# Performance work log

Measured on AMD Instinct MI355X. Metric: run time of the kernel, lower is better.

Reference implementation:

```python
import jax, jax.numpy as jnp
import numpy as np

B, N, D, H, HID, EN = 2, 4096, 128, 4, 32, 16
ALPHA = 0.2           # LeakyReLU slope
NEG = -9e15           # masked_fill value from the original code


def setup_inputs() -> dict:
    key = jax.random.key(0)
    ks = jax.random.split(key, 6)
    fea = jax.random.normal(ks[0], (B, N, D), dtype=jnp.float32)
    # binary dense adjacency (regulon x gene), square here so narrow() is identity
    adj = jax.random.randint(ks[1], (B, N, N), 0, 2).astype(jnp.float32)
    # per-head GAT params (xavier-ish scale)
    W_heads = jax.random.normal(ks[2], (H, D, HID), dtype=jnp.float32) * 0.1
    a_heads = jax.random.normal(ks[3], (H, 2 * HID, 1), dtype=jnp.float32) * 0.1
    W_last = jax.random.normal(ks[4], (H * HID, EN), dtype=jnp.float32) * 0.1
    a_last = jax.random.normal(ks[5], (2 * EN, 1), dtype=jnp.float32) * 0.1
    return {"fea_mats": fea, "adj_mats": adj, "W_heads": W_heads,
            "a_heads": a_heads, "W_last": W_last, "a_last": a_last}


def _gat_layer(x, adj, W, a, concat):
    # x: [N, d_in], adj: [nr, N], W: [d_in, out], a: [2*out, 1]
    out_dim = W.shape[1]
    wh = x @ W                                   # [N, out]
    nr = adj.shape[0]
    wh1 = wh[:nr] @ a[:out_dim]                  # [nr, 1]
    wh2 = wh @ a[out_dim:]                       # [N, 1]
    e = jax.nn.leaky_relu(wh1 + wh2.T, ALPHA)    # [nr, N]
    # _prepare_attentions: mask by adj, weight by adj, fill zeros with -9e15
    att = jnp.where(adj != 0, e * adj, 0.0)
    att = jnp.where(att == 0, NEG, att)
    att = jax.nn.softmax(att, axis=1)
    # the original detaches attention via a numpy roundtrip
    att = jax.lax.stop_gradient(att)
    res = att @ wh                               # [nr, out]
    return jax.nn.elu(res) if concat else res


def reference(fea_mats, adj_mats, W_heads, a_heads, W_last, a_last):
    def per_sample(x, adj):
        # multi-head attention layers (concat=True), vmapped over heads
        heads = jax.vmap(lambda W, a: _gat_layer(x, adj, W, a, True))(W_heads, a_heads)  # [H, N, HID]
        xcat = jnp.transpose(heads, (1, 0, 2)).reshape(x.shape[0], H * HID)  # torch.cat(dim=1)
        nr = adj.shape[0]
        out = _gat_layer(xcat, adj[:, :nr], W_last, a_last, False)  # adj.narrow(1,0,nr)
        return jax.nn.elu(out)  # [N, EN]
    return jax.vmap(per_sample)(fea_mats, adj_mats)  # [B, N, EN]
```

## Files before the change

kernel.cpp:

```cpp
#include <hip/hip_runtime.h>
#include <hip/hip_bf16.h>
#include <stdint.h>

#define B_ 2
#define N_ 4096
#define D_ 128
#define H_ 4
#define HID_ 32
#define EN_ 16
#define ALPHA_ 0.2f
#define S1_ 4
#define S2_ 4
#define LOG2E_ 1.4426950408889634f

typedef __attribute__((ext_vector_type(8))) _Float16 f16x8;
typedef __attribute__((ext_vector_type(4))) float f32x4;
typedef __attribute__((ext_vector_type(8))) unsigned short u16x8;

__device__ __forceinline__ unsigned short f2h(float v) {
    _Float16 h = (_Float16)v;
    return *(unsigned short*)&h;
}

__global__ __launch_bounds__(256) void maskc_kernel(
    const float* __restrict__ adj, unsigned long long* __restrict__ mask)
{
    const int b = blockIdx.y;
    const int i = blockIdx.x * 4 + (threadIdx.x >> 6);
    const int lane = threadIdx.x & 63;
    const float* ar = adj + ((size_t)b * N_ + i) * N_;
    unsigned long long* mrow = mask + ((size_t)b * N_ + i) * 64;
#pragma unroll 4
    for (int c = 0; c < 16; ++c) {
        float4 v = *(const float4*)(ar + c * 256 + lane * 4);
        unsigned long long b0 = __ballot(v.x != 0.f);
        unsigned long long b1 = __ballot(v.y != 0.f);
        unsigned long long b2 = __ballot(v.z != 0.f);
        unsigned long long b3 = __ballot(v.w != 0.f);
        if (lane == 0) {
            ulonglong2 w01 = {b0, b1}, w23 = {b2, b3};
            *(ulonglong2*)(mrow + c * 4) = w01;
            *(ulonglong2*)(mrow + c * 4 + 2) = w23;
        }
    }
}

__global__ __launch_bounds__(256) void proj1_kernel(
    const float* __restrict__ fea, const float* __restrict__ Wh,
    const float* __restrict__ a_heads,
    float* __restrict__ wh1, float* __restrict__ wh2,
    float* __restrict__ cmax1, unsigned short* __restrict__ whTt)
{
    __shared__ float xs[64][132];
    __shared__ float WT[32][132];
    __shared__ float Wa[2][128];
    __shared__ float as_[2 * HID_];
    __shared__ unsigned short ts[32 * 64];
    __shared__ float rmax[64];
    const int b = blockIdx.z, h = blockIdx.y, i0 = blockIdx.x * 64, tid = threadIdx.x;
    const float* Wp = Wh + (size_t)h * D_ * HID_;
    for (int l = tid; l < 1024; l += 256) {
        float4 w4 = *(const float4*)(Wp + l * 4);
        int k = l >> 3, d = (l & 7) * 4;
        WT[d][k] = w4.x; WT[d + 1][k] = w4.y; WT[d + 2][k] = w4.z; WT[d + 3][k] = w4.w;
    }
    if (tid < 2 * HID_) as_[tid] = a_heads[h * 2 * HID_ + tid];
    const float* xp = fea + ((size_t)b * N_ + i0) * D_;
    for (int l = tid; l < 2048; l += 256) {
        int r = l >> 5, k4 = (l & 31) * 4;
        *(float4*)&xs[r][k4] = *(const float4*)(xp + r * D_ + k4);
    }
    __syncthreads();
    {
        const int k = tid & 127, j = tid >> 7;
        const float* wr = Wp + k * HID_;
        const float* aw = &as_[j * HID_];
        float s = 0.f;
#pragma unroll
        for (int d = 0; d < HID_; d += 4) {
            float4 w4 = *(const float4*)(wr + d);
            s += w4.x * aw[d] + w4.y * aw[d + 1] + w4.z * aw[d + 2] + w4.w * aw[d + 3];
        }
        Wa[j][k] = s;
    }
    const int rg = (tid >> 4) * 4, c = tid & 15;
    float a0[4] = {0.f, 0.f, 0.f, 0.f}, a1[4] = {0.f, 0.f, 0.f, 0.f};
#pragma unroll 8
    for (int k = 0; k < D_; k += 4) {
        float4 w0 = *(float4*)&WT[c][k];
        float4 w1 = *(float4*)&WT[c + 16][k];
#pragma unroll
        for (int i = 0; i < 4; ++i) {
            float4 x4 = *(float4*)&xs[rg + i][k];
            a0[i] += x4.x * w0.x + x4.y * w0.y + x4.z * w0.z + x4.w * w0.w;
            a1[i] += x4.x * w1.x + x4.y * w1.y + x4.z * w1.z + x4.w * w1.w;
        }
    }
#pragma unroll
    for (int i = 0; i < 4; ++i) {
        ts[c * 64 + rg + i] = f2h(a0[i]);
        ts[(c + 16) * 64 + rg + i] = f2h(a1[i]);
    }
    __syncthreads();
    {
        const int row = tid >> 2, q = tid & 3;
        float d1 = 0.f, d2 = 0.f;
#pragma unroll
        for (int k = q * 32; k < q * 32 + 32; k += 4) {
            float4 x4 = *(float4*)&xs[row][k];
            float4 u = *(float4*)&Wa[0][k];
            float4 v = *(float4*)&Wa[1][k];
            d1 += x4.x * u.x + x4.y * u.y + x4.z * u.z + x4.w * u.w;
            d2 += x4.x * v.x + x4.y * v.y + x4.z * v.z + x4.w * v.w;
        }
        d1 += __shfl_xor(d1, 1); d1 += __shfl_xor(d1, 2);
        d2 += __shfl_xor(d2, 1); d2 += __shfl_xor(d2, 2);
        if (q == 0) {
            const size_t o = (size_t)(b * H_ + h) * N_ + i0 + row;
            wh1[o] = d1 * LOG2E_;
            wh2[o] = d2 * LOG2E_;
            rmax[row] = d2 * LOG2E_;
        }
    }
    __syncthreads();
    {
        unsigned short* dst = whTt + ((size_t)(b * H_ + h) * 64 + blockIdx.x) * 2048;
        *(u16x8*)(dst + tid * 8) = *(u16x8*)&ts[tid * 8];
    }
    if (tid < 64) {
        float mx = rmax[tid];
#pragma unroll
        for (int off = 32; off; off >>= 1) mx = fmaxf(mx, __shfl_xor(mx, off));
        if (tid == 0) cmax1[(size_t)(b * H_ + h) * 64 + blockIdx.x] = mx;
    }
}

__global__ __launch_bounds__(256, 4) void attn1_kernel(
    const unsigned long long* __restrict__ mask, const unsigned short* __restrict__ whT,
    const float* __restrict__ wh1, const float* __restrict__ wh2,
    const float* __restrict__ cmax1,
    float* __restrict__ x2p, float* __restrict__ l1p)
{
    __shared__ unsigned long long mask_s[32][17];
    const int b = blockIdx.z, split = blockIdx.y, i0 = blockIdx.x * 32;
    const int tid = threadIdx.x, lane = tid & 63, h = tid >> 6;
    const int m = lane & 15, quad = lane >> 4;
    {
        const int r = tid >> 3, w = (tid & 7) * 2;
        ulonglong2 mw = *(const ulonglong2*)(mask + ((size_t)b * N_ + i0 + r) * 64
                                             + split * 16 + w);
        mask_s[r][w] = mw.x; mask_s[r][w + 1] = mw.y;
    }
    const float* cm = cmax1 + (size_t)(b * H_ + h) * 64;
    float Mh = cm[lane];
#pragma unroll
    for (int off = 32; off; off >>= 1) Mh = fmaxf(Mh, __shfl_xor(Mh, off));
    const size_t bhN = (size_t)(b * H_ + h) * N_;
    const float w1r0 = wh1[bhN + i0 + m];
    const float w1r1 = wh1[bhN + i0 + 16 + m];
    const float sb0 = w1r0 + Mh, sb1 = w1r1 + Mh;
    const float mr0 = fmaxf(sb0, ALPHA_ * sb0);
    const float mr1 = fmaxf(sb1, ALPHA_ * sb1);
    const float* wvb = wh2 + bhN + split * 1024 + quad * 8;
    const unsigned short* bpb = whT + (size_t)(b * H_ + h) * 131072
                              + (size_t)split * 16 * 2048 + m * 64 + quad * 8;
    f32x4 a00 = {0.f,0.f,0.f,0.f}, a01 = {0.f,0.f,0.f,0.f}, a02 = {0.f,0.f,0.f,0.f};
    f32x4 a10 = {0.f,0.f,0.f,0.f}, a11 = {0.f,0.f,0.f,0.f}, a12 = {0.f,0.f,0.f,0.f};
    f16x8 ones;
#pragma unroll
    for (int q = 0; q < 8; ++q) ones[q] = (_Float16)1.0f;
    __syncthreads();

    for (int c = 0; c < 4; ++c) {
        const unsigned long long P0 = mask_s[m][c*4+0], P1 = mask_s[m][c*4+1];
        const unsigned long long P2 = mask_s[m][c*4+2], P3 = mask_s[m][c*4+3];
        const unsigned long long Q0 = mask_s[m+16][c*4+0], Q1 = mask_s[m+16][c*4+1];
        const unsigned long long Q2 = mask_s[m+16][c*4+2], Q3 = mask_s[m+16][c*4+3];
#pragma unroll
        for (int q4 = 0; q4 < 4; ++q4) {
            const int t = c * 4 + q4;
            const unsigned short* bp = bpb + (size_t)t * 2048;
            f16x8 b00 = *(const f16x8*)bp;
            f16x8 b10 = *(const f16x8*)(bp + 32);
            f16x8 b01 = *(const f16x8*)(bp + 1024);
            f16x8 b11 = *(const f16x8*)(bp + 1056);
            const float* nw = wvb + t * 64;
            float4 u0 = *(const float4*)nw;
            float4 u1 = *(const float4*)(nw + 4);
            float4 v0 = *(const float4*)(nw + 32);
            float4 v1 = *(const float4*)(nw + 36);
#pragma unroll
            for (int ks = 0; ks < 2; ++ks) {
                const int sh = 16 * q4 + 8 * ks + 2 * quad;
                float wv8[8];
                if (ks == 0) { *(float4*)&wv8[0] = u0; *(float4*)&wv8[4] = u1; }
                else         { *(float4*)&wv8[0] = v0; *(float4*)&wv8[4] = v1; }
                const unsigned int gp0 = (unsigned int)(P0 >> sh) & 3u;
                const unsigned int gp1 = (unsigned int)(P1 >> sh) & 3u;
                const unsigned int gp2 = (unsigned int)(P2 >> sh) & 3u;
                const unsigned int gp3 = (unsigned int)(P3 >> sh) & 3u;
                const unsigned int gq0 = (unsigned int)(Q0 >> sh) & 3u;
                const unsigned int gq1 = (unsigned int)(Q1 >> sh) & 3u;
                const unsigned int gq2 = (unsigned int)(Q2 >> sh) & 3u;
                const unsigned int gq3 = (unsigned int)(Q3 >> sh) & 3u;
                f16x8 af0, af1;
#pragma unroll
                for (int qq = 0; qq < 4; ++qq) {
                    float r0p[2], r1p[2];
#pragma unroll
                    for (int cc = 0; cc < 2; ++cc) {
                        const int jj = qq * 2 + cc;
                        const unsigned int bsel = 1u << (jj >> 2);
                        const unsigned int gp = (jj&3)==0?gp0:(jj&3)==1?gp1:(jj&3)==2?gp2:gp3;
                        const unsigned int gq = (jj&3)==0?gq0:(jj&3)==1?gq1:(jj&3)==2?gq2:gq3;
                        float s0 = w1r0 + wv8[jj];
                        float e0 = fmaxf(s0, ALPHA_ * s0);
                        float t0 = ((gp & bsel) == 0u || s0 == 0.f) ? -1e38f : (e0 - mr0);
                        r0p[cc] = __builtin_amdgcn_exp2f(t0);
                        float s1 = w1r1 + wv8[jj];
                        float e1 = fmaxf(s1, ALPHA_ * s1);
                        float t1 = ((gq & bsel) == 0u || s1 == 0.f) ? -1e38f : (e1 - mr1);
                        r1p[cc] = __builtin_amdgcn_exp2f(t1);
                    }
                    auto pr0 = __builtin_amdgcn_cvt_pkrtz(r0p[0], r0p[1]);
                    af0[qq*2] = (_Float16)pr0[0]; af0[qq*2+1] = (_Float16)pr0[1];
                    auto pr1 = __builtin_amdgcn_cvt_pkrtz(r1p[0], r1p[1]);
                    af1[qq*2] = (_Float16)pr1[0]; af1[qq*2+1] = (_Float16)pr1[1];
                }
                f16x8 bb0 = ks ? b10 : b00;
                f16x8 bb1 = ks ? b11 : b01;
                a00 = __builtin_amdgcn_mfma_f32_16x16x32_f16(af0, bb0, a00, 0, 0, 0);
                a01 = __builtin_amdgcn_mfma_f32_16x16x32_f16(af0, bb1, a01, 0, 0, 0);
                a02 = __builtin_amdgcn_mfma_f32_16x16x32_f16(af0, ones, a02, 0, 0, 0);
                a10 = __builtin_amdgcn_mfma_f32_16x16x32_f16(af1, bb0, a10, 0, 0, 0);
                a11 = __builtin_amdgcn_mfma_f32_16x16x32_f16(af1, bb1, a11, 0, 0, 0);
                a12 = __builtin_amdgcn_mfma_f32_16x16x32_f16(af1, ones, a12, 0, 0, 0);
            }
        }
    }
    float* xp = x2p + (((size_t)split * B_ + b) * N_ + i0) * D_ + h * HID_;
#pragma unroll
    for (int reg = 0; reg < 4; ++reg) {
        const int row = quad * 4 + reg;
        xp[(size_t)row * D_ + m] = a00[reg];
        xp[(size_t)row * D_ + 16 + m] = a01[reg];
        xp[(size_t)(row + 16) * D_ + m] = a10[reg];
        xp[(size_t)(row + 16) * D_ + 16 + m] = a11[reg];
    }
    if (m == 0) {
        float* lp = l1p + (((size_t)split * B_ + b) * N_ + i0) * H_ + h;
#pragma unroll
        for (int reg = 0; reg < 4; ++reg) {
            lp[(size_t)(quad * 4 + reg) * H_] = a02[reg];
            lp[(size_t)(quad * 4 + reg + 16) * H_] = a12[reg];
        }
    }
}

__global__ __launch_bounds__(256) void proj2_kernel(
    const float* __restrict__ x2p, const float* __restrict__ l1p,
    const float* __restrict__ Wl, const float* __restrict__ a_last,
    float* __restrict__ wh1b, float* __restrict__ wh2b,
    float* __restrict__ cmax2, unsigned short* __restrict__ whT2t)
{
    __shared__ float Ws[D_ * EN_];
    __shared__ float xs[16][D_];
    __shared__ float as_[2 * EN_];
    __shared__ unsigned short ts[EN_][16];
    __shared__ float rmax[16];
    const int b = blockIdx.y, i0 = blockIdx.x * 16, tid = threadIdx.x;
    for (int idx = tid * 4; idx < D_ * EN_; idx += 1024)
        *(float4*)&Ws[idx] = *(const float4*)(Wl + idx);
    if (tid < 2 * EN_) as_[tid] = a_last[tid];
    for (int idx = tid * 4; idx < 16 * D_; idx += 1024) {
        const int r = idx >> 7, hd = idx & 127, h = hd >> 5;
        float4 v = {0.f, 0.f, 0.f, 0.f};
        float l = 0.f;
#pragma unroll
        for (int s = 0; s < S1_; ++s) {
            const size_t gi = ((size_t)s * B_ + b) * N_ + i0 + r;
            float4 p = *(const float4*)(x2p + gi * D_ + hd);
            v.x += p.x; v.y += p.y; v.z += p.z; v.w += p.w;
            l += l1p[gi * H_ + h];
        }
        float linv = 1.f / fmaxf(l, 1e-30f);
        float o0 = v.x * linv, o1 = v.y * linv, o2 = v.z * linv, o3 = v.w * linv;
        xs[r][hd]     = o0 > 0.f ? o0 : expm1f(o0);
        xs[r][hd + 1] = o1 > 0.f ? o1 : expm1f(o1);
        xs[r][hd + 2] = o2 > 0.f ? o2 : expm1f(o2);
        xs[r][hd + 3] = o3 > 0.f ? o3 : expm1f(o3);
    }
    __syncthreads();
    const int r = tid >> 4, e = tid & 15;
    float acc = 0.f;
#pragma unroll 8
    for (int k = 0; k < D_; ++k) acc += xs[r][k] * Ws[k * EN_ + e];
    ts[e][r] = f2h(acc);
    float d1 = acc * as_[e], d2 = acc * as_[EN_ + e];
#pragma unroll
    for (int off = 8; off; off >>= 1) {
        d1 += __shfl_xor(d1, off);
        d2 += __shfl_xor(d2, off);
    }
    d1 *= LOG2E_; d2 *= LOG2E_;
    if (e == 0) {
        wh1b[(size_t)b * N_ + i0 + r] = d1;
        wh2b[(size_t)b * N_ + i0 + r] = d2;
        rmax[r] = d2;
    }
    __syncthreads();
    if (tid < EN_) {
        unsigned short* dst = whT2t + (size_t)b * 65536
                            + (i0 >> 6) * 1024 + tid * 64 + (i0 & 63);
        *(u16x8*)dst = *(u16x8*)&ts[tid][0];
        *(u16x8*)(dst + 8) = *(u16x8*)&ts[tid][8];
    }
    if (tid == 0) {
        float mx = rmax[0];
#pragma unroll
        for (int k = 1; k < 16; ++k) mx = fmaxf(mx, rmax[k]);
        cmax2[(size_t)b * 256 + blockIdx.x] = mx;
    }
}

__global__ __launch_bounds__(256) void attn2_kernel(
    const unsigned long long* __restrict__ mask, const unsigned short* __restrict__ whT2,
    const float* __restrict__ wh1b, const float* __restrict__ wh2b,
    const float* __restrict__ cmax2,
    float* __restrict__ outp, float* __restrict__ outlp)
{
    __shared__ unsigned long long mask_s[16][18];
    __shared__ float accred[4][16][17];
    __shared__ float lred[4][16];
    const int b = blockIdx.z, split = blockIdx.y, i0 = blockIdx.x * 16;
    const int tid = threadIdx.x, lane = tid & 63, wv = tid >> 6;
    const int m = lane & 15, quad = lane >> 4;
    mask_s[tid >> 4][tid & 15] =
        mask[((size_t)b * N_ + i0 + (tid >> 4)) * 64 + split * 16 + (tid & 15)];
    const float* cm = cmax2 + (size_t)b * 256;
    float4 c0 = *(const float4*)(cm + lane * 4);
    float Mh = fmaxf(fmaxf(c0.x, c0.y), fmaxf(c0.z, c0.w));
#pragma unroll
    for (int off = 32; off; off >>= 1) Mh = fmaxf(Mh, __shfl_xor(Mh, off));
    const float w1r = wh1b[(size_t)b * N_ + i0 + m];
    const float sbound = w1r + Mh;
    const float mr = fmaxf(sbound, ALPHA_ * sbound);
    const float* w2g = wh2b + (size_t)b * N_;
    const unsigned short* wTg = whT2 + (size_t)b * 65536;
    f32x4 acc = {0.f, 0.f, 0.f, 0.f}, acc2 = {0.f, 0.f, 0.f, 0.f};
    f16x8 ones;
#pragma unroll
    for (int q = 0; q < 8; ++q) ones[q] = (_Float16)1.0f;
    const int jt0 = split * (N_ / S2_);
    __syncthreads();
    unsigned long long W0 = mask_s[m][wv * 4 + 0], W1 = mask_s[m][wv * 4 + 1];
    unsigned long long W2 = mask_s[m][wv * 4 + 2], W3 = mask_s[m][wv * 4 + 3];

    const unsigned short* wTb = wTg + (size_t)(split * 16 + wv * 4) * 1024 + m * 64 + quad * 8;
    const float* wvb = w2g + jt0 + wv * 256 + quad * 8;
#pragma unroll
    for (int q4 = 0; q4 < 4; ++q4) {
        const unsigned short* bp = wTb + (size_t)q4 * 1024;
        f16x8 cb0 = *(const f16x8*)(bp);
        f16x8 cb1 = *(const f16x8*)(bp + 32);
        const float* nw = wvb + q4 * 64;
        float4 cu0 = *(const float4*)(nw);
        float4 cu1 = *(const float4*)(nw + 4);
        float4 cv0 = *(const float4*)(nw + 32);
        float4 cv1 = *(const float4*)(nw + 36);
#pragma unroll
        for (int ks = 0; ks < 2; ++ks) {
            const int sh = 16 * q4 + 8 * ks + 2 * quad;
            unsigned int g0 = (unsigned int)(W0 >> sh) & 3u;
            unsigned int g1 = (unsigned int)(W1 >> sh) & 3u;
            unsigned int g2 = (unsigned int)(W2 >> sh) & 3u;
            unsigned int g3 = (unsigned int)(W3 >> sh) & 3u;
            float wv8[8];
            if (ks == 0) { *(float4*)&wv8[0] = cu0; *(float4*)&wv8[4] = cu1; }
            else         { *(float4*)&wv8[0] = cv0; *(float4*)&wv8[4] = cv1; }
            f16x8 af;
#pragma unroll
            for (int q = 0; q < 4; ++q) {
                float p2[2];
#pragma unroll
                for (int cc = 0; cc < 2; ++cc) {
                    const int jj = q * 2 + cc;
                    unsigned int gw = (jj & 3) == 0 ? g0 : (jj & 3) == 1 ? g1
                                    : (jj & 3) == 2 ? g2 : g3;
                    unsigned int bit = gw & (1u << (jj >> 2));
                    float s = w1r + wv8[jj];
                    float e = fmaxf(s, ALPHA_ * s);
                    float tt = (bit == 0u || s == 0.f) ? -1e38f : (e - mr);
                    p2[cc] = __builtin_amdgcn_exp2f(tt);
                }
                auto pr = __builtin_amdgcn_cvt_pkrtz(p2[0], p2[1]);
                af[q * 2] = (_Float16)pr[0]; af[q * 2 + 1] = (_Float16)pr[1];
            }
            acc = __builtin_amdgcn_mfma_f32_16x16x32_f16(af, ks ? cb1 : cb0, acc, 0, 0, 0);
            acc2 = __builtin_amdgcn_mfma_f32_16x16x32_f16(af, ones, acc2, 0, 0, 0);
        }
    }
#pragma unroll
    for (int reg = 0; reg < 4; ++reg)
        accred[wv][quad * 4 + reg][m] = acc[reg];
    if (m == 0) {
#pragma unroll
        for (int reg = 0; reg < 4; ++reg) lred[wv][quad * 4 + reg] = acc2[reg];
    }
    __syncthreads();
    const int row = tid >> 4, col = tid & 15;
    float s = accred[0][row][col] + accred[1][row][col]
            + accred[2][row][col] + accred[3][row][col];
    outp[(((size_t)split * B_ + b) * N_ + i0 + row) * EN_ + col] = s;
    if (tid < 16) {
        float l = lred[0][tid] + lred[1][tid] + lred[2][tid] + lred[3][tid];
        outlp[((size_t)split * B_ + b) * N_ + i0 + tid] = l;
    }
}

__global__ __launch_bounds__(256) void finalize2_kernel(
    const float* __restrict__ outp, const float* __restrict__ outlp,
    float* __restrict__ out)
{
    const int id = blockIdx.x * 256 + threadIdx.x;
    const int gi = id >> 4;
    float num = 0.f, l = 0.f;
#pragma unroll
    for (int s = 0; s < S2_; ++s) {
        num += outp[(size_t)s * B_ * N_ * EN_ + id];
        l   += outlp[(size_t)s * B_ * N_ + gi];
    }
    float v = num / fmaxf(l, 1e-30f);
    out[id] = v > 0.f ? v : expm1f(v);
}

extern "C" void kernel_launch(void* const* d_in, const int* in_sizes, int n_in,
                              void* d_out, int out_size, void* d_ws, size_t ws_size,
                              hipStream_t stream)
{
    const float* fea = (const float*)d_in[0];
    const float* adj = (const float*)d_in[1];
    const float* Wh  = (const float*)d_in[2];
    const float* ah  = (const float*)d_in[3];
    const float* Wl  = (const float*)d_in[4];
    const float* al  = (const float*)d_in[5];

    float* p = (float*)d_ws;
    float* wh1   = p;  p += (size_t)B_ * H_ * N_;
    float* wh2   = p;  p += (size_t)B_ * H_ * N_;
    float* wh1b  = p;  p += (size_t)B_ * N_;
    float* wh2b  = p;  p += (size_t)B_ * N_;
    float* cmax1 = p;  p += (size_t)B_ * H_ * 64;
    float* cmax2 = p;  p += (size_t)B_ * 256;
    float* l1p   = p;  p += (size_t)S1_ * B_ * N_ * H_;
    float* x2p   = p;  p += (size_t)S1_ * B_ * N_ * D_;
    float* outp  = p;  p += (size_t)S2_ * B_ * N_ * EN_;
    float* outlp = p;  p += (size_t)S2_ * B_ * N_;
    unsigned long long* mask = (unsigned long long*)p;
    unsigned short* whTt  = (unsigned short*)(mask + (size_t)B_ * N_ * 64);
    unsigned short* whT2t = whTt + (size_t)B_ * H_ * 131072;

    maskc_kernel<<<dim3(N_ / 4, B_), 256, 0, stream>>>(adj, mask);
    proj1_kernel<<<dim3(N_ / 64, H_, B_), 256, 0, stream>>>(fea, Wh, ah,
                                                            wh1, wh2, cmax1, whTt);
    attn1_kernel<<<dim3(N_ / 32, S1_, B_), 256, 0, stream>>>(mask, whTt, wh1, wh2, cmax1,
                                                             x2p, l1p);
    proj2_kernel<<<dim3(N_ / 16, B_), 256, 0, stream>>>(x2p, l1p, Wl, al,
                                                        wh1b, wh2b, cmax2, whT2t);
    attn2_kernel<<<dim3(N_ / 16, S2_, B_), 256, 0, stream>>>(mask, whT2t, wh1b, wh2b, cmax2,
                                                             outp, outlp);
    finalize2_kernel<<<(B_ * N_ * EN_) / 256, 256, 0, stream>>>(outp, outlp, (float*)d_out);
}
```

Measured before the change: 287.6 us.

## Merge mask and projection kernels; give attn2 blocks two 16-row tiles

The mask-compression kernel and the first projection kernel become one launch: the first 2048 blocks build the mask bitmaps and the rest compute the per-head projections on 32-row tiles (cmax1 doubles to 128 entries per head). This removes one launch and lets the two independent jobs run side by side. attn2 now handles 32 rows per block with two MFMA accumulator sets, so each loaded B fragment and wh2 value serves twice as many rows, and its launch bound asks for 4 blocks per CU. The cost is more registers in attn2 and half as many attn2 blocks.

```diff
diff --git a/kernel.cpp b/kernel.cpp
--- a/kernel.cpp
+++ b/kernel.cpp
@@ -22,42 +22,45 @@
     return *(unsigned short*)&h;
 }
 
-__global__ __launch_bounds__(256) void maskc_kernel(
-    const float* __restrict__ adj, unsigned long long* __restrict__ mask)
-{
-    const int b = blockIdx.y;
-    const int i = blockIdx.x * 4 + (threadIdx.x >> 6);
-    const int lane = threadIdx.x & 63;
-    const float* ar = adj + ((size_t)b * N_ + i) * N_;
-    unsigned long long* mrow = mask + ((size_t)b * N_ + i) * 64;
-#pragma unroll 4
-    for (int c = 0; c < 16; ++c) {
-        float4 v = *(const float4*)(ar + c * 256 + lane * 4);
-        unsigned long long b0 = __ballot(v.x != 0.f);
-        unsigned long long b1 = __ballot(v.y != 0.f);
-        unsigned long long b2 = __ballot(v.z != 0.f);
-        unsigned long long b3 = __ballot(v.w != 0.f);
-        if (lane == 0) {
-            ulonglong2 w01 = {b0, b1}, w23 = {b2, b3};
-            *(ulonglong2*)(mrow + c * 4) = w01;
-            *(ulonglong2*)(mrow + c * 4 + 2) = w23;
-        }
-    }
-}
-
-__global__ __launch_bounds__(256) void proj1_kernel(
+__global__ __launch_bounds__(256) void prep_kernel(
+    const float* __restrict__ adj, unsigned long long* __restrict__ mask,
     const float* __restrict__ fea, const float* __restrict__ Wh,
     const float* __restrict__ a_heads,
     float* __restrict__ wh1, float* __restrict__ wh2,
     float* __restrict__ cmax1, unsigned short* __restrict__ whTt)
 {
-    __shared__ float xs[64][132];
+    __shared__ float xs[32][132];
     __shared__ float WT[32][132];
     __shared__ float Wa[2][128];
     __shared__ float as_[2 * HID_];
-    __shared__ unsigned short ts[32 * 64];
-    __shared__ float rmax[64];
-    const int b = blockIdx.z, h = blockIdx.y, i0 = blockIdx.x * 64, tid = threadIdx.x;
+    __shared__ unsigned short ts[32][32];
+    __shared__ float rmax[32];
+    const int tid = threadIdx.x;
+
+    if (blockIdx.x < 2048) {
+        const int b = blockIdx.x >> 10, ib = blockIdx.x & 1023;
+        const int i = ib * 4 + (tid >> 6);
+        const int lane = tid & 63;
+        const float* ar = adj + ((size_t)b * N_ + i) * N_;
+        unsigned long long* mrow = mask + ((size_t)b * N_ + i) * 64;
+#pragma unroll 4
+        for (int c = 0; c < 16; ++c) {
+            float4 v = *(const float4*)(ar + c * 256 + lane * 4);
+            unsigned long long b0 = __ballot(v.x != 0.f);
+            unsigned long long b1 = __ballot(v.y != 0.f);
+            unsigned long long b2 = __ballot(v.z != 0.f);
+            unsigned long long b3 = __ballot(v.w != 0.f);
+            if (lane == 0) {
+                ulonglong2 w01 = {b0, b1}, w23 = {b2, b3};
+                *(ulonglong2*)(mrow + c * 4) = w01;
+                *(ulonglong2*)(mrow + c * 4 + 2) = w23;
+            }
+        }
+        return;
+    }
+    const int l0 = blockIdx.x - 2048;
+    const int ib = l0 & 127, h = (l0 >> 7) & 3, b = l0 >> 9;
+    const int i0 = ib * 32;
     const float* Wp = Wh + (size_t)h * D_ * HID_;
     for (int l = tid; l < 1024; l += 256) {
         float4 w4 = *(const float4*)(Wp + l * 4);
@@ -66,7 +69,7 @@
     }
     if (tid < 2 * HID_) as_[tid] = a_heads[h * 2 * HID_ + tid];
     const float* xp = fea + ((size_t)b * N_ + i0) * D_;
-    for (int l = tid; l < 2048; l += 256) {
+    for (int l = tid; l < 1024; l += 256) {
         int r = l >> 5, k4 = (l & 31) * 4;
         *(float4*)&xs[r][k4] = *(const float4*)(xp + r * D_ + k4);
     }
@@ -83,38 +86,38 @@
         }
         Wa[j][k] = s;
     }
-    const int rg = (tid >> 4) * 4, c = tid & 15;
-    float a0[4] = {0.f, 0.f, 0.f, 0.f}, a1[4] = {0.f, 0.f, 0.f, 0.f};
+    const int c = tid & 15, rg = (tid >> 4) * 2;
+    float a0[2] = {0.f, 0.f}, a1[2] = {0.f, 0.f};
 #pragma unroll 8
     for (int k = 0; k < D_; k += 4) {
         float4 w0 = *(float4*)&WT[c][k];
         float4 w1 = *(float4*)&WT[c + 16][k];
 #pragma unroll
-        for (int i = 0; i < 4; ++i) {
+        for (int i = 0; i < 2; ++i) {
             float4 x4 = *(float4*)&xs[rg + i][k];
             a0[i] += x4.x * w0.x + x4.y * w0.y + x4.z * w0.z + x4.w * w0.w;
             a1[i] += x4.x * w1.x + x4.y * w1.y + x4.z * w1.z + x4.w * w1.w;
         }
     }
 #pragma unroll
-    for (int i = 0; i < 4; ++i) {
-        ts[c * 64 + rg + i] = f2h(a0[i]);
-        ts[(c + 16) * 64 + rg + i] = f2h(a1[i]);
+    for (int i = 0; i < 2; ++i) {
+        ts[c][rg + i] = f2h(a0[i]);
+        ts[c + 16][rg + i] = f2h(a1[i]);
     }
     __syncthreads();
     {
-        const int row = tid >> 2, q = tid & 3;
+        const int row = tid >> 3, q = tid & 7;
         float d1 = 0.f, d2 = 0.f;
 #pragma unroll
-        for (int k = q * 32; k < q * 32 + 32; k += 4) {
+        for (int k = q * 16; k < q * 16 + 16; k += 4) {
             float4 x4 = *(float4*)&xs[row][k];
             float4 u = *(float4*)&Wa[0][k];
             float4 v = *(float4*)&Wa[1][k];
             d1 += x4.x * u.x + x4.y * u.y + x4.z * u.z + x4.w * u.w;
             d2 += x4.x * v.x + x4.y * v.y + x4.z * v.z + x4.w * v.w;
         }
-        d1 += __shfl_xor(d1, 1); d1 += __shfl_xor(d1, 2);
-        d2 += __shfl_xor(d2, 1); d2 += __shfl_xor(d2, 2);
+        d1 += __shfl_xor(d1, 1); d1 += __shfl_xor(d1, 2); d1 += __shfl_xor(d1, 4);
+        d2 += __shfl_xor(d2, 1); d2 += __shfl_xor(d2, 2); d2 += __shfl_xor(d2, 4);
         if (q == 0) {
             const size_t o = (size_t)(b * H_ + h) * N_ + i0 + row;
             wh1[o] = d1 * LOG2E_;
@@ -123,15 +126,17 @@
         }
     }
     __syncthreads();
-    {
-        unsigned short* dst = whTt + ((size_t)(b * H_ + h) * 64 + blockIdx.x) * 2048;
-        *(u16x8*)(dst + tid * 8) = *(u16x8*)&ts[tid * 8];
-    }
-    if (tid < 64) {
+    if (tid < 128) {
+        const int d = tid >> 2, part = (tid & 3) * 8;
+        unsigned short* dst = whTt + ((size_t)(b * H_ + h) * 64 + (i0 >> 6)) * 2048
+                            + d * 64 + (i0 & 63) + part;
+        *(u16x8*)dst = *(u16x8*)&ts[d][part];
+    }
+    if (tid < 32) {
         float mx = rmax[tid];
 #pragma unroll
-        for (int off = 32; off; off >>= 1) mx = fmaxf(mx, __shfl_xor(mx, off));
-        if (tid == 0) cmax1[(size_t)(b * H_ + h) * 64 + blockIdx.x] = mx;
+        for (int off = 16; off; off >>= 1) mx = fmaxf(mx, __shfl_xor(mx, off));
+        if (tid == 0) cmax1[(size_t)(b * H_ + h) * 128 + ib] = mx;
     }
 }
 
@@ -151,8 +156,8 @@
                                              + split * 16 + w);
         mask_s[r][w] = mw.x; mask_s[r][w + 1] = mw.y;
     }
-    const float* cm = cmax1 + (size_t)(b * H_ + h) * 64;
-    float Mh = cm[lane];
+    const float* cm = cmax1 + (size_t)(b * H_ + h) * 128;
+    float Mh = fmaxf(cm[lane], cm[lane + 64]);
 #pragma unroll
     for (int off = 32; off; off >>= 1) Mh = fmaxf(Mh, __shfl_xor(Mh, off));
     const size_t bhN = (size_t)(b * H_ + h) * N_;
@@ -323,96 +328,124 @@
     }
 }
 
-__global__ __launch_bounds__(256) void attn2_kernel(
+__global__ __launch_bounds__(256, 4) void attn2_kernel(
     const unsigned long long* __restrict__ mask, const unsigned short* __restrict__ whT2,
     const float* __restrict__ wh1b, const float* __restrict__ wh2b,
     const float* __restrict__ cmax2,
     float* __restrict__ outp, float* __restrict__ outlp)
 {
-    __shared__ unsigned long long mask_s[16][18];
-    __shared__ float accred[4][16][17];
-    __shared__ float lred[4][16];
-    const int b = blockIdx.z, split = blockIdx.y, i0 = blockIdx.x * 16;
+    __shared__ unsigned long long mask_s[32][17];
+    __shared__ float accred[4][32][17];
+    __shared__ float lred[4][32];
+    const int b = blockIdx.z, split = blockIdx.y, i0 = blockIdx.x * 32;
     const int tid = threadIdx.x, lane = tid & 63, wv = tid >> 6;
     const int m = lane & 15, quad = lane >> 4;
-    mask_s[tid >> 4][tid & 15] =
-        mask[((size_t)b * N_ + i0 + (tid >> 4)) * 64 + split * 16 + (tid & 15)];
+    {
+        const int r = tid >> 3, w = (tid & 7) * 2;
+        ulonglong2 mw = *(const ulonglong2*)(mask + ((size_t)b * N_ + i0 + r) * 64
+                                             + split * 16 + w);
+        mask_s[r][w] = mw.x; mask_s[r][w + 1] = mw.y;
+    }
     const float* cm = cmax2 + (size_t)b * 256;
     float4 c0 = *(const float4*)(cm + lane * 4);
     float Mh = fmaxf(fmaxf(c0.x, c0.y), fmaxf(c0.z, c0.w));
 #pragma unroll
     for (int off = 32; off; off >>= 1) Mh = fmaxf(Mh, __shfl_xor(Mh, off));
-    const float w1r = wh1b[(size_t)b * N_ + i0 + m];
-    const float sbound = w1r + Mh;
-    const float mr = fmaxf(sbound, ALPHA_ * sbound);
-    const float* w2g = wh2b + (size_t)b * N_;
-    const unsigned short* wTg = whT2 + (size_t)b * 65536;
-    f32x4 acc = {0.f, 0.f, 0.f, 0.f}, acc2 = {0.f, 0.f, 0.f, 0.f};
+    const float w1r0 = wh1b[(size_t)b * N_ + i0 + m];
+    const float w1r1 = wh1b[(size_t)b * N_ + i0 + 16 + m];
+    const float sb0 = w1r0 + Mh, sb1 = w1r1 + Mh;
+    const float mr0 = fmaxf(sb0, ALPHA_ * sb0);
+    const float mr1 = fmaxf(sb1, ALPHA_ * sb1);
+    const unsigned short* wTb = whT2 + (size_t)b * 65536
+                              + (size_t)(split * 16 + wv * 4) * 1024 + m * 64 + quad * 8;
+    const float* wvb = wh2b + (size_t)b * N_ + split * 1024 + wv * 256 + quad * 8;
+    f32x4 a0 = {0.f,0.f,0.f,0.f}, a1 = {0.f,0.f,0.f,0.f};
+    f32x4 l0 = {0.f,0.f,0.f,0.f}, l1 = {0.f,0.f,0.f,0.f};
     f16x8 ones;
 #pragma unroll
     for (int q = 0; q < 8; ++q) ones[q] = (_Float16)1.0f;
-    const int jt0 = split * (N_ / S2_);
-    __syncthreads();
-    unsigned long long W0 = mask_s[m][wv * 4 + 0], W1 = mask_s[m][wv * 4 + 1];
-    unsigned long long W2 = mask_s[m][wv * 4 + 2], W3 = mask_s[m][wv * 4 + 3];
-
-    const unsigned short* wTb = wTg + (size_t)(split * 16 + wv * 4) * 1024 + m * 64 + quad * 8;
-    const float* wvb = w2g + jt0 + wv * 256 + quad * 8;
+    __syncthreads();
+    const unsigned long long P0 = mask_s[m][wv*4+0], P1 = mask_s[m][wv*4+1];
+    const unsigned long long P2 = mask_s[m][wv*4+2], P3 = mask_s[m][wv*4+3];
+    const unsigned long long Q0 = mask_s[m+16][wv*4+0], Q1 = mask_s[m+16][wv*4+1];
+    const unsigned long long Q2 = mask_s[m+16][wv*4+2], Q3 = mask_s[m+16][wv*4+3];
 #pragma unroll
     for (int q4 = 0; q4 < 4; ++q4) {
         const unsigned short* bp = wTb + (size_t)q4 * 1024;
         f16x8 cb0 = *(const f16x8*)(bp);
         f16x8 cb1 = *(const f16x8*)(bp + 32);
         const float* nw = wvb + q4 * 64;
-        float4 cu0 = *(const float4*)(nw);
-        float4 cu1 = *(const float4*)(nw + 4);
-        float4 cv0 = *(const float4*)(nw + 32);
-        float4 cv1 = *(const float4*)(nw + 36);
+        float4 u0 = *(const float4*)(nw);
+        float4 u1 = *(const float4*)(nw + 4);
+        float4 v0 = *(const float4*)(nw + 32);
+        float4 v1 = *(const float4*)(nw + 36);
 #pragma unroll
         for (int ks = 0; ks < 2; ++ks) {
             const int sh = 16 * q4 + 8 * ks + 2 * quad;
-            unsigned int g0 = (unsigned int)(W0 >> sh) & 3u;
-            unsigned int g1 = (unsigned int)(W1 >> sh) & 3u;
-            unsigned int g2 = (unsigned int)(W2 >> sh) & 3u;
-            unsigned int g3 = (unsigned int)(W3 >> sh) & 3u;
             float wv8[8];
-            if (ks == 0) { *(float4*)&wv8[0] = cu0; *(float4*)&wv8[4] = cu1; }
-            else         { *(float4*)&wv8[0] = cv0; *(float4*)&wv8[4] = cv1; }
-            f16x8 af;
-#pragma unroll
-            for (int q = 0; q < 4; ++q) {
-                float p2[2];
+            if (ks == 0) { *(float4*)&wv8[0] = u0; *(float4*)&wv8[4] = u1; }
+            else         { *(float4*)&wv8[0] = v0; *(float4*)&wv8[4] = v1; }
+            const unsigned int gp0 = (unsigned int)(P0 >> sh) & 3u;
+            const unsigned int gp1 = (unsigned int)(P1 >> sh) & 3u;
+            const unsigned int gp2 = (unsigned int)(P2 >> sh) & 3u;
+            const unsigned int gp3 = (unsigned int)(P3 >> sh) & 3u;
+            const unsigned int gq0 = (unsigned int)(Q0 >> sh) & 3u;
+            const unsigned int gq1 = (unsigned int)(Q1 >> sh) & 3u;
+            const unsigned int gq2 = (unsigned int)(Q2 >> sh) & 3u;
+            const unsigned int gq3 = (unsigned int)(Q3 >> sh) & 3u;
+            f16x8 af0, af1;
+#pragma unroll
+            for (int qq = 0; qq < 4; ++qq) {
+                float r0p[2], r1p[2];
 #pragma unroll
                 for (int cc = 0; cc < 2; ++cc) {
-                    const int jj = q * 2 + cc;
-                    unsigned int gw = (jj & 3) == 0 ? g0 : (jj & 3) == 1 ? g1
-                                    : (jj & 3) == 2 ? g2 : g3;
-                    unsigned int bit = gw & (1u << (jj >> 2));
-                    float s = w1r + wv8[jj];
-                    float e = fmaxf(s, ALPHA_ * s);
-                    float tt = (bit == 0u || s == 0.f) ? -1e38f : (e - mr);
-                    p2[cc] = __builtin_amdgcn_exp2f(tt);
+                    const int jj = qq * 2 + cc;
+                    const unsigned int bsel = 1u << (jj >> 2);
+                    const unsigned int gp = (jj&3)==0?gp0:(jj&3)==1?gp1:(jj&3)==2?gp2:gp3;
+                    const unsigned int gq = (jj&3)==0?gq0:(jj&3)==1?gq1:(jj&3)==2?gq2:gq3;
+                    float s0 = w1r0 + wv8[jj];
+                    float e0 = fmaxf(s0, ALPHA_ * s0);
+                    float t0 = ((gp & bsel) == 0u || s0 == 0.f) ? -1e38f : (e0 - mr0);
+                    r0p[cc] = __builtin_amdgcn_exp2f(t0);
+                    float s1 = w1r1 + wv8[jj];
+                    float e1 = fmaxf(s1, ALPHA_ * s1);
+                    float t1 = ((gq & bsel) == 0u || s1 == 0.f) ? -1e38f : (e1 - mr1);
+                    r1p[cc] = __builtin_amdgcn_exp2f(t1);
                 }
-                auto pr = __builtin_amdgcn_cvt_pkrtz(p2[0], p2[1]);
-                af[q * 2] = (_Float16)pr[0]; af[q * 2 + 1] = (_Float16)pr[1];
+                auto pr0 = __builtin_amdgcn_cvt_pkrtz(r0p[0], r0p[1]);
+                af0[qq*2] = (_Float16)pr0[0]; af0[qq*2+1] = (_Float16)pr0[1];
+                auto pr1 = __builtin_amdgcn_cvt_pkrtz(r1p[0], r1p[1]);
+                af1[qq*2] = (_Float16)pr1[0]; af1[qq*2+1] = (_Float16)pr1[1];
             }
-            acc = __builtin_amdgcn_mfma_f32_16x16x32_f16(af, ks ? cb1 : cb0, acc, 0, 0, 0);
-            acc2 = __builtin_amdgcn_mfma_f32_16x16x32_f16(af, ones, acc2, 0, 0, 0);
-        }
-    }
-#pragma unroll
-    for (int reg = 0; reg < 4; ++reg)
-        accred[wv][quad * 4 + reg][m] = acc[reg];
+            f16x8 bb = ks ? cb1 : cb0;
+            a0 = __builtin_amdgcn_mfma_f32_16x16x32_f16(af0, bb, a0, 0, 0, 0);
+            l0 = __builtin_amdgcn_mfma_f32_16x16x32_f16(af0, ones, l0, 0, 0, 0);
+            a1 = __builtin_amdgcn_mfma_f32_16x16x32_f16(af1, bb, a1, 0, 0, 0);
+            l1 = __builtin_amdgcn_mfma_f32_16x16x32_f16(af1, ones, l1, 0, 0, 0);
+        }
+    }
+#pragma unroll
+    for (int reg = 0; reg < 4; ++reg) {
+        accred[wv][quad * 4 + reg][m] = a0[reg];
+        accred[wv][quad * 4 + reg + 16][m] = a1[reg];
+    }
     if (m == 0) {
 #pragma unroll
-        for (int reg = 0; reg < 4; ++reg) lred[wv][quad * 4 + reg] = acc2[reg];
+        for (int reg = 0; reg < 4; ++reg) {
+            lred[wv][quad * 4 + reg] = l0[reg];
+            lred[wv][quad * 4 + reg + 16] = l1[reg];
+        }
     }
     __syncthreads();
     const int row = tid >> 4, col = tid & 15;
-    float s = accred[0][row][col] + accred[1][row][col]
-            + accred[2][row][col] + accred[3][row][col];
-    outp[(((size_t)split * B_ + b) * N_ + i0 + row) * EN_ + col] = s;
-    if (tid < 16) {
+    float s0 = accred[0][row][col] + accred[1][row][col]
+             + accred[2][row][col] + accred[3][row][col];
+    float s1 = accred[0][row + 16][col] + accred[1][row + 16][col]
+             + accred[2][row + 16][col] + accred[3][row + 16][col];
+    float* op = outp + (((size_t)split * B_ + b) * N_ + i0) * EN_;
+    op[(size_t)row * EN_ + col] = s0;
+    op[(size_t)(row + 16) * EN_ + col] = s1;
+    if (tid < 32) {
         float l = lred[0][tid] + lred[1][tid] + lred[2][tid] + lred[3][tid];
         outlp[((size_t)split * B_ + b) * N_ + i0 + tid] = l;
     }
@@ -450,7 +483,7 @@
     float* wh2   = p;  p += (size_t)B_ * H_ * N_;
     float* wh1b  = p;  p += (size_t)B_ * N_;
     float* wh2b  = p;  p += (size_t)B_ * N_;
-    float* cmax1 = p;  p += (size_t)B_ * H_ * 64;
+    float* cmax1 = p;  p += (size_t)B_ * H_ * 128;
     float* cmax2 = p;  p += (size_t)B_ * 256;
     float* l1p   = p;  p += (size_t)S1_ * B_ * N_ * H_;
     float* x2p   = p;  p += (size_t)S1_ * B_ * N_ * D_;
@@ -460,14 +493,13 @@
     unsigned short* whTt  = (unsigned short*)(mask + (size_t)B_ * N_ * 64);
     unsigned short* whT2t = whTt + (size_t)B_ * H_ * 131072;
 
-    maskc_kernel<<<dim3(N_ / 4, B_), 256, 0, stream>>>(adj, mask);
-    proj1_kernel<<<dim3(N_ / 64, H_, B_), 256, 0, stream>>>(fea, Wh, ah,
-                                                            wh1, wh2, cmax1, whTt);
+    prep_kernel<<<2048 + B_ * H_ * 128, 256, 0, stream>>>(adj, mask, fea, Wh, ah,
+                                                          wh1, wh2, cmax1, whTt);
     attn1_kernel<<<dim3(N_ / 32, S1_, B_), 256, 0, stream>>>(mask, whTt, wh1, wh2, cmax1,
                                                              x2p, l1p);
     proj2_kernel<<<dim3(N_ / 16, B_), 256, 0, stream>>>(x2p, l1p, Wl, al,
                                                         wh1b, wh2b, cmax2, whT2t);
-    attn2_kernel<<<dim3(N_ / 16, S2_, B_), 256, 0, stream>>>(mask, whT2t, wh1b, wh2b, cmax2,
+    attn2_kernel<<<dim3(N_ / 32, S2_, B_), 256, 0, stream>>>(mask, whT2t, wh1b, wh2b, cmax2,
                                                              outp, outlp);
     finalize2_kernel<<<(B_ * N_ * EN_) / 256, 256, 0, stream>>>(outp, outlp, (float*)d_out);
 }
```

Result: no change. 282.8 us (-1.7%).
